# Kernel optimization log

Hardware: AMD Instinct MI355X
Metric: run time of the kernel (lower is better)

The kernel has to match this reference:

```python
import jax, jax.numpy as jnp
import numpy as np

B, N, D_IN, D_OUT, E = 16, 16384, 128, 128, 65536
LN_EPS = 1e-5


def setup_inputs() -> dict:
    key = jax.random.key(0)
    k1, k2, k3, k4 = jax.random.split(key, 4)
    x = jax.random.normal(k1, (B, N, D_IN), dtype=jnp.float32)
    edge_index = jax.random.randint(k2, (2, E), 0, N, dtype=jnp.int64)
    W_self = jax.random.normal(k3, (D_OUT, D_IN), dtype=jnp.float32) / np.sqrt(D_IN)
    W_neigh = jax.random.normal(k4, (D_OUT, D_IN), dtype=jnp.float32) / np.sqrt(D_IN)
    return {
        "x": x,
        "edge_index": edge_index,
        "batch_size": B,
        "W_self": W_self,
        "W_neigh": W_neigh,
        "bias": jnp.zeros((D_OUT,), jnp.float32),
        "gamma": jnp.ones((D_OUT,), jnp.float32),
        "beta": jnp.zeros((D_OUT,), jnp.float32),
    }


def reference(x, edge_index, batch_size, W_self, W_neigh, bias, gamma, beta):
    b, n, d = x.shape
    src, dst = edge_index[0], edge_index[1]
    # expand edge index for disjoint batched graphs: add per-graph node offsets
    offsets = (jnp.arange(batch_size, dtype=src.dtype) * n)[:, None]  # [B,1]
    src_e = (src[None, :] + offsets).reshape(-1)  # [B*E]
    dst_e = (dst[None, :] + offsets).reshape(-1)
    x_flat = x.reshape(batch_size * n, d)
    # scatter-sum neighbor features and degrees, then mean
    agg = jax.ops.segment_sum(x_flat[src_e], dst_e, num_segments=batch_size * n)
    deg = jax.ops.segment_sum(jnp.ones_like(dst_e, dtype=x_flat.dtype), dst_e,
                              num_segments=batch_size * n)
    neigh = agg / jnp.maximum(deg, 1.0)[:, None]
    out = x_flat @ W_self.T + neigh @ W_neigh.T + bias  # [B*N, D_OUT]
    # LayerNorm over last dim
    mu = jnp.mean(out, axis=-1, keepdims=True)
    var = jnp.mean(jnp.square(out - mu), axis=-1, keepdims=True)
    out = (out - mu) * jax.lax.rsqrt(var + LN_EPS) * gamma + beta
    out = jax.nn.relu(out)
    return out.reshape(batch_size, n, -1)
```

## Files before the change

kernel.cpp:

```cpp
#include <hip/hip_runtime.h>
#include <hip/hip_bf16.h>
#include <stdint.h>

#define B_ 16
#define N_ 16384
#define D_ 128
#define E_ 65536

typedef __attribute__((ext_vector_type(8))) __bf16 bf16x8;
typedef __attribute__((ext_vector_type(4))) float f32x4;

__device__ __forceinline__ uint16_t f2bf(float f) {
    union { float f; uint32_t u; } v;
    v.f = f;
    uint32_t u = v.u;
    uint32_t r = (u + 0x7fffu + ((u >> 16) & 1u)) >> 16;
    return (uint16_t)r;
}

__global__ void k_detect(const int* __restrict__ ei, int* __restrict__ flag) {
    __shared__ int nz;
    if (threadIdx.x == 0) nz = 0;
    __syncthreads();
    if (ei[2 * threadIdx.x + 1] != 0) atomicAdd(&nz, 1);
    __syncthreads();
    if (threadIdx.x == 0) *flag = (nz == 0) ? 1 : 0;
}


__global__ void k_count(const int* __restrict__ ei, const int* __restrict__ flag,
                        int* __restrict__ deg) {
    int e = blockIdx.x * 256 + threadIdx.x;
    int f = *flag;
    int d = f ? ei[2 * (E_ + e)] : ei[E_ + e];
    atomicAdd(&deg[d], 1);
}

__global__ void k_scan(const int* __restrict__ deg, int* __restrict__ off,
                       int* __restrict__ cur) {
    __shared__ int part[256];
    __shared__ int pre[257];
    int t = threadIdx.x;
    int base = t * 64;
    int s = 0;
    for (int i = 0; i < 64; i++) s += deg[base + i];
    part[t] = s;
    __syncthreads();
    if (t == 0) {
        int run = 0;
        for (int i = 0; i < 256; i++) { pre[i] = run; run += part[i]; }
        pre[256] = run;
    }
    __syncthreads();
    int run = pre[t];
    for (int i = 0; i < 64; i++) {
        off[base + i] = run;
        cur[base + i] = run;
        run += deg[base + i];
    }
    if (t == 0) off[N_] = pre[256];
}

__global__ void k_fill(const int* __restrict__ ei, const int* __restrict__ flag,
                       int* __restrict__ cur, int* __restrict__ adj) {
    int e = blockIdx.x * 256 + threadIdx.x;
    int f = *flag;
    int s = f ? ei[2 * e] : ei[e];
    int d = f ? ei[2 * (E_ + e)] : ei[E_ + e];
    int p = atomicAdd(&cur[d], 1);
    adj[p] = s;
}

__global__ void k_pack(const float* __restrict__ wself,
                       const float* __restrict__ wneigh,
                       uint16_t* __restrict__ wpack) {
    int g = blockIdx.x * 256 + threadIdx.x;
    int j = g & 7;
    int lane = (g >> 3) & 63;
    int nt = (g >> 9) & 7;
    int ks = g >> 12;
    int k = ks * 32 + (lane >> 4) * 8 + j;
    int n = nt * 16 + (lane & 15);
    float v = (k < 128) ? wself[n * 128 + k] : wneigh[n * 128 + (k - 128)];
    wpack[g] = f2bf(v);
}


__global__ __launch_bounds__(256) void k_main(
    const float* __restrict__ x,
    const int* __restrict__ off,
    const int* __restrict__ adj,
    const uint16_t* __restrict__ wpack,
    const float* __restrict__ bias,
    const float* __restrict__ gamma_,
    const float* __restrict__ beta_,
    float* __restrict__ out) {
    __shared__ __align__(16) unsigned char smem[33792];
    __shared__ float prm[3][128];
    uint16_t* As = (uint16_t*)smem;
    float* Cs = (float*)smem;

    int t = threadIdx.x;
    int b = blockIdx.x & 15;
    int tile = blockIdx.x >> 4;
    int node0 = tile * 64;

    if (t < 128) {
        prm[0][t] = bias[t];
        prm[1][t] = gamma_[t];
        prm[2][t] = beta_[t];
    }

    int r = t >> 2;
    int q = t & 3;
    int node = node0 + r;
    const size_t xrow_base = ((size_t)b * N_ + node) * D_;
    int mt = r >> 4, m = r & 15;

    {
        const float4* xv = (const float4*)(x + xrow_base);
#pragma unroll
        for (int c = 0; c < 4; c++) {
            float4 a0 = xv[q * 8 + 2 * c + 0];
            float4 a1 = xv[q * 8 + 2 * c + 1];
            float f[8] = {a0.x, a0.y, a0.z, a0.w, a1.x, a1.y, a1.z, a1.w};
            uint32_t pk[4];
#pragma unroll
            for (int p = 0; p < 4; p++)
                pk[p] = (uint32_t)f2bf(f[2 * p]) | ((uint32_t)f2bf(f[2 * p + 1]) << 16);
            int kc = q * 4 + c;
            int ks = kc >> 2, qd = kc & 3;
            uint4 v = make_uint4(pk[0], pk[1], pk[2], pk[3]);
            *(uint4*)&As[(((ks * 4 + mt) * 64) + qd * 16 + m) * 8] = v;
        }
    }

    {
        int o0 = off[node], o1 = off[node + 1];
        float acc[32];
#pragma unroll
        for (int i = 0; i < 32; i++) acc[i] = 0.f;
        for (int e = o0; e < o1; e++) {
            int nbr = adj[e];
            const float4* nv = (const float4*)(x + ((size_t)b * N_ + nbr) * D_);
#pragma unroll
            for (int cc = 0; cc < 8; cc++) {
                float4 v = nv[q * 8 + cc];
                acc[cc * 4 + 0] += v.x;
                acc[cc * 4 + 1] += v.y;
                acc[cc * 4 + 2] += v.z;
                acc[cc * 4 + 3] += v.w;
            }
        }
        float scale = 1.f / fmaxf((float)(o1 - o0), 1.f);
#pragma unroll
        for (int c = 0; c < 4; c++) {
            uint32_t pk[4];
#pragma unroll
            for (int p = 0; p < 4; p++) {
                uint16_t lo = f2bf(acc[c * 8 + 2 * p + 0] * scale);
                uint16_t hi = f2bf(acc[c * 8 + 2 * p + 1] * scale);
                pk[p] = (uint32_t)lo | ((uint32_t)hi << 16);
            }
            int kc = 16 + q * 4 + c;
            int ks = kc >> 2, qd = kc & 3;
            uint4 v = make_uint4(pk[0], pk[1], pk[2], pk[3]);
            *(uint4*)&As[(((ks * 4 + mt) * 64) + qd * 16 + m) * 8] = v;
        }
    }

    __syncthreads();

    int wv = t >> 6;
    int lane = t & 63;
    f32x4 accv[4][2];
#pragma unroll
    for (int i = 0; i < 4; i++)
#pragma unroll
        for (int j = 0; j < 2; j++) {
            f32x4 z = {0.f, 0.f, 0.f, 0.f};
            accv[i][j] = z;
        }

    const uint4* wp = (const uint4*)wpack;
#pragma unroll
    for (int ks = 0; ks < 8; ks++) {
        uint4 b0u = wp[(ks * 8 + 2 * wv + 0) * 64 + lane];
        uint4 b1u = wp[(ks * 8 + 2 * wv + 1) * 64 + lane];
        bf16x8 bf0 = __builtin_bit_cast(bf16x8, b0u);
        bf16x8 bf1 = __builtin_bit_cast(bf16x8, b1u);
#pragma unroll
        for (int mtt = 0; mtt < 4; mtt++) {
            bf16x8 a = *(const bf16x8*)&As[((ks * 4 + mtt) * 64 + lane) * 8];
            accv[mtt][0] = __builtin_amdgcn_mfma_f32_16x16x32_bf16(a, bf0, accv[mtt][0], 0, 0, 0);
            accv[mtt][1] = __builtin_amdgcn_mfma_f32_16x16x32_bf16(a, bf1, accv[mtt][1], 0, 0, 0);
        }
    }

    __syncthreads();

#pragma unroll
    for (int mtt = 0; mtt < 4; mtt++)
#pragma unroll
        for (int ntl = 0; ntl < 2; ntl++)
#pragma unroll
            for (int rg = 0; rg < 4; rg++) {
                int row = mtt * 16 + (lane >> 4) * 4 + rg;
                int col = (2 * wv + ntl) * 16 + (lane & 15);
                Cs[row * 132 + (col >> 5) * 33 + (col & 31)] = accv[mtt][ntl][rg];
            }

    __syncthreads();

    {
        float s1 = 0.f, s2 = 0.f;
#pragma unroll
        for (int i = 0; i < 32; i++) {
            float v = Cs[r * 132 + q * 33 + i] + prm[0][q * 32 + i];
            s1 += v;
            s2 += v * v;
        }
        s1 += __shfl_xor(s1, 1, 64);
        s2 += __shfl_xor(s2, 1, 64);
        s1 += __shfl_xor(s1, 2, 64);
        s2 += __shfl_xor(s2, 2, 64);
        float mu = s1 * (1.f / 128.f);
        float var = s2 * (1.f / 128.f) - mu * mu;
        float rstd = rsqrtf(var + 1e-5f);

        float* orow = out + xrow_base;
#pragma unroll
        for (int c = 0; c < 8; c++) {
            float4 o;
            float tmp[4];
#pragma unroll
            for (int j = 0; j < 4; j++) {
                int i0 = c * 4 + j;
                int d0 = q * 32 + i0;
                float v = Cs[r * 132 + q * 33 + i0] + prm[0][d0];
                tmp[j] = fmaxf((v - mu) * rstd * prm[1][d0] + prm[2][d0], 0.f);
            }
            o.x = tmp[0]; o.y = tmp[1]; o.z = tmp[2]; o.w = tmp[3];
            *(float4*)&orow[q * 32 + c * 4] = o;
        }
    }
}

extern "C" void kernel_launch(void* const* d_in, const int* in_sizes, int n_in,
                              void* d_out, int out_size, void* d_ws, size_t ws_size,
                              hipStream_t stream) {
    (void)in_sizes; (void)n_in; (void)out_size; (void)ws_size;
    const float* x      = (const float*)d_in[0];
    const int*   ei     = (const int*)d_in[1];
    const float* wself  = (const float*)d_in[3];
    const float* wneigh = (const float*)d_in[4];
    const float* bias   = (const float*)d_in[5];
    const float* gma    = (const float*)d_in[6];
    const float* bta    = (const float*)d_in[7];
    float* out = (float*)d_out;

    char* ws = (char*)d_ws;
    int* deg        = (int*)(ws);
    int* off        = (int*)(ws + 65536);
    int* cur        = (int*)(ws + 131584);
    int* adj        = (int*)(ws + 197120);
    uint16_t* wpack = (uint16_t*)(ws + 459264);
    int* flag       = (int*)(ws + 524800);

    hipMemsetAsync(deg, 0, N_ * sizeof(int), stream);
    k_detect<<<1, 256, 0, stream>>>(ei, flag);
    k_count<<<E_ / 256, 256, 0, stream>>>(ei, flag, deg);
    k_scan<<<1, 256, 0, stream>>>(deg, off, cur);
    k_fill<<<E_ / 256, 256, 0, stream>>>(ei, flag, cur, adj);
    k_pack<<<128, 256, 0, stream>>>(wself, wneigh, wpack);
    k_main<<<B_ * (N_ / 64), 256, 0, stream>>>(x, off, adj, wpack, bias, gma, bta, out);
}
```

Measured before the change: 394.1 us.

## Split neighbor aggregation into coalesced kernel staging bf16 means in output buffer

Moves the mean-neighbor gather out of the GEMM kernel into a dedicated kernel where 32 lanes cooperatively read each neighbor row, writing bf16 means into the unused half of each output row for the GEMM kernel to consume. Also fuses degree counting with weight packing, replaces the detect kernel with a wave ballot, and parallelizes the prefix scan. It aims for better-coalesced, higher-occupancy gathers and fewer launches, at the cost of an extra scratch round-trip through the output buffer.

```diff
diff --git a/kernel.cpp b/kernel.cpp
--- a/kernel.cpp
+++ b/kernel.cpp
@@ -18,83 +18,119 @@
     return (uint16_t)r;
 }
 
-__global__ void k_detect(const int* __restrict__ ei, int* __restrict__ flag) {
-    __shared__ int nz;
-    if (threadIdx.x == 0) nz = 0;
-    __syncthreads();
-    if (ei[2 * threadIdx.x + 1] != 0) atomicAdd(&nz, 1);
-    __syncthreads();
-    if (threadIdx.x == 0) *flag = (nz == 0) ? 1 : 0;
-}
-
-
-__global__ void k_count(const int* __restrict__ ei, const int* __restrict__ flag,
-                        int* __restrict__ deg) {
-    int e = blockIdx.x * 256 + threadIdx.x;
-    int f = *flag;
-    int d = f ? ei[2 * (E_ + e)] : ei[E_ + e];
-    atomicAdd(&deg[d], 1);
+__device__ __forceinline__ bool ei_is64(const int* __restrict__ ei, int t) {
+    int w = ei[2 * (t & 63) + 1];
+    return __ballot(w != 0) == 0ull;
+}
+
+__global__ void k_cntpack(const int* __restrict__ ei,
+                          const float* __restrict__ wself,
+                          const float* __restrict__ wneigh,
+                          int* __restrict__ deg,
+                          uint16_t* __restrict__ wpack) {
+    int t = threadIdx.x;
+    int bid = blockIdx.x;
+    if (bid < 256) {
+        bool is64 = ei_is64(ei, t);
+        int e = bid * 256 + t;
+        int d = is64 ? ei[2 * (E_ + e)] : ei[E_ + e];
+        atomicAdd(&deg[d], 1);
+    } else {
+        int g = (bid - 256) * 256 + t;
+        int j = g & 7;
+        int lane = (g >> 3) & 63;
+        int nt = (g >> 9) & 7;
+        int ks = g >> 12;
+        int k = ks * 32 + (lane >> 4) * 8 + j;
+        int n = nt * 16 + (lane & 15);
+        float v = (k < 128) ? wself[n * 128 + k] : wneigh[n * 128 + (k - 128)];
+        wpack[g] = f2bf(v);
+    }
 }
 
 __global__ void k_scan(const int* __restrict__ deg, int* __restrict__ off,
                        int* __restrict__ cur) {
-    __shared__ int part[256];
-    __shared__ int pre[257];
-    int t = threadIdx.x;
-    int base = t * 64;
+    __shared__ int ps[256];
+    int t = threadIdx.x;
+    int vals[64];
+    const int4* dv = (const int4*)(deg + t * 64);
     int s = 0;
-    for (int i = 0; i < 64; i++) s += deg[base + i];
-    part[t] = s;
-    __syncthreads();
-    if (t == 0) {
-        int run = 0;
-        for (int i = 0; i < 256; i++) { pre[i] = run; run += part[i]; }
-        pre[256] = run;
-    }
-    __syncthreads();
-    int run = pre[t];
+#pragma unroll
+    for (int i = 0; i < 16; i++) {
+        int4 v = dv[i];
+        vals[4 * i + 0] = v.x; vals[4 * i + 1] = v.y;
+        vals[4 * i + 2] = v.z; vals[4 * i + 3] = v.w;
+        s += v.x + v.y + v.z + v.w;
+    }
+    ps[t] = s;
+    __syncthreads();
+#pragma unroll
+    for (int st = 1; st < 256; st <<= 1) {
+        int add = (t >= st) ? ps[t - st] : 0;
+        __syncthreads();
+        ps[t] += add;
+        __syncthreads();
+    }
+    int run = ps[t] - s;
+#pragma unroll
     for (int i = 0; i < 64; i++) {
-        off[base + i] = run;
-        cur[base + i] = run;
-        run += deg[base + i];
-    }
-    if (t == 0) off[N_] = pre[256];
-}
-
-__global__ void k_fill(const int* __restrict__ ei, const int* __restrict__ flag,
-                       int* __restrict__ cur, int* __restrict__ adj) {
-    int e = blockIdx.x * 256 + threadIdx.x;
-    int f = *flag;
-    int s = f ? ei[2 * e] : ei[e];
-    int d = f ? ei[2 * (E_ + e)] : ei[E_ + e];
+        off[t * 64 + i] = run;
+        cur[t * 64 + i] = run;
+        run += vals[i];
+    }
+    if (t == 255) off[N_] = run;
+}
+
+__global__ void k_fill(const int* __restrict__ ei, int* __restrict__ cur,
+                       int* __restrict__ adj) {
+    int t = threadIdx.x;
+    bool is64 = ei_is64(ei, t);
+    int e = blockIdx.x * 256 + t;
+    int s = is64 ? ei[2 * e] : ei[e];
+    int d = is64 ? ei[2 * (E_ + e)] : ei[E_ + e];
     int p = atomicAdd(&cur[d], 1);
     adj[p] = s;
 }
 
-__global__ void k_pack(const float* __restrict__ wself,
-                       const float* __restrict__ wneigh,
-                       uint16_t* __restrict__ wpack) {
-    int g = blockIdx.x * 256 + threadIdx.x;
-    int j = g & 7;
-    int lane = (g >> 3) & 63;
-    int nt = (g >> 9) & 7;
-    int ks = g >> 12;
-    int k = ks * 32 + (lane >> 4) * 8 + j;
-    int n = nt * 16 + (lane & 15);
-    float v = (k < 128) ? wself[n * 128 + k] : wneigh[n * 128 + (k - 128)];
-    wpack[g] = f2bf(v);
-}
-
+__global__ __launch_bounds__(256) void k_agg(const float* __restrict__ x,
+                                             const int* __restrict__ off,
+                                             const int* __restrict__ adj,
+                                             unsigned char* __restrict__ scratch) {
+    int t = threadIdx.x;
+    int g = blockIdx.x & 15;
+    int chunk = blockIdx.x >> 4;
+    int hw = t >> 5, l = t & 31;
+    int node = chunk * 8 + hw;
+    int o0 = off[node], o1 = off[node + 1];
+    const float* xg = x + (size_t)g * N_ * D_;
+    float ax = 0.f, ay = 0.f, az = 0.f, aw = 0.f;
+    int e = o0;
+    for (; e + 1 < o1; e += 2) {
+        int s0 = adj[e], s1 = adj[e + 1];
+        float4 v0 = *(const float4*)(xg + (size_t)s0 * D_ + l * 4);
+        float4 v1 = *(const float4*)(xg + (size_t)s1 * D_ + l * 4);
+        ax += v0.x + v1.x; ay += v0.y + v1.y;
+        az += v0.z + v1.z; aw += v0.w + v1.w;
+    }
+    if (e < o1) {
+        int s0 = adj[e];
+        float4 v0 = *(const float4*)(xg + (size_t)s0 * D_ + l * 4);
+        ax += v0.x; ay += v0.y; az += v0.z; aw += v0.w;
+    }
+    float sc = 1.f / fmaxf((float)(o1 - o0), 1.f);
+    uint32_t p0 = (uint32_t)f2bf(ax * sc) | ((uint32_t)f2bf(ay * sc) << 16);
+    uint32_t p1 = (uint32_t)f2bf(az * sc) | ((uint32_t)f2bf(aw * sc) << 16);
+    uint2 pv; pv.x = p0; pv.y = p1;
+    *(uint2*)(scratch + ((size_t)g * N_ + node) * 512 + 256 + l * 8) = pv;
+}
 
 __global__ __launch_bounds__(256) void k_main(
     const float* __restrict__ x,
-    const int* __restrict__ off,
-    const int* __restrict__ adj,
     const uint16_t* __restrict__ wpack,
     const float* __restrict__ bias,
     const float* __restrict__ gamma_,
     const float* __restrict__ beta_,
-    float* __restrict__ out) {
+    float* out) {
     __shared__ __align__(16) unsigned char smem[33792];
     __shared__ float prm[3][128];
     uint16_t* As = (uint16_t*)smem;
@@ -136,35 +172,13 @@
     }
 
     {
-        int o0 = off[node], o1 = off[node + 1];
-        float acc[32];
-#pragma unroll
-        for (int i = 0; i < 32; i++) acc[i] = 0.f;
-        for (int e = o0; e < o1; e++) {
-            int nbr = adj[e];
-            const float4* nv = (const float4*)(x + ((size_t)b * N_ + nbr) * D_);
-#pragma unroll
-            for (int cc = 0; cc < 8; cc++) {
-                float4 v = nv[q * 8 + cc];
-                acc[cc * 4 + 0] += v.x;
-                acc[cc * 4 + 1] += v.y;
-                acc[cc * 4 + 2] += v.z;
-                acc[cc * 4 + 3] += v.w;
-            }
-        }
-        float scale = 1.f / fmaxf((float)(o1 - o0), 1.f);
+        const uint4* nv = (const uint4*)((const unsigned char*)out +
+                                         ((size_t)b * N_ + node) * 512 + 256);
 #pragma unroll
         for (int c = 0; c < 4; c++) {
-            uint32_t pk[4];
-#pragma unroll
-            for (int p = 0; p < 4; p++) {
-                uint16_t lo = f2bf(acc[c * 8 + 2 * p + 0] * scale);
-                uint16_t hi = f2bf(acc[c * 8 + 2 * p + 1] * scale);
-                pk[p] = (uint32_t)lo | ((uint32_t)hi << 16);
-            }
+            uint4 v = nv[q * 4 + c];
             int kc = 16 + q * 4 + c;
             int ks = kc >> 2, qd = kc & 3;
-            uint4 v = make_uint4(pk[0], pk[1], pk[2], pk[3]);
             *(uint4*)&As[(((ks * 4 + mt) * 64) + qd * 16 + m) * 8] = v;
         }
     }
@@ -265,13 +279,11 @@
     int* cur        = (int*)(ws + 131584);
     int* adj        = (int*)(ws + 197120);
     uint16_t* wpack = (uint16_t*)(ws + 459264);
-    int* flag       = (int*)(ws + 524800);
 
     hipMemsetAsync(deg, 0, N_ * sizeof(int), stream);
-    k_detect<<<1, 256, 0, stream>>>(ei, flag);
-    k_count<<<E_ / 256, 256, 0, stream>>>(ei, flag, deg);
+    k_cntpack<<<384, 256, 0, stream>>>(ei, wself, wneigh, deg, wpack);
     k_scan<<<1, 256, 0, stream>>>(deg, off, cur);
-    k_fill<<<E_ / 256, 256, 0, stream>>>(ei, flag, cur, adj);
-    k_pack<<<128, 256, 0, stream>>>(wself, wneigh, wpack);
-    k_main<<<B_ * (N_ / 64), 256, 0, stream>>>(x, off, adj, wpack, bias, gma, bta, out);
-}
+    k_fill<<<E_ / 256, 256, 0, stream>>>(ei, cur, adj);
+    k_agg<<<B_ * N_ / 8, 256, 0, stream>>>(x, off, adj, (unsigned char*)out);
+    k_main<<<B_ * (N_ / 64), 256, 0, stream>>>(x, wpack, bias, gma, bta, out);
+}
```

New measurement: 388.7 us. Within noise of the previous version (-1.4%).
